# Kernel optimization log

Hardware: AMD Instinct MI355X
Metric: run time of the kernel (lower is better)

## Reference

```python
import jax, jax.numpy as jnp
import numpy as np

B = 1048576
IN, H = 16, 12


def _xavier(key, shape):
    fan_out, fan_in = shape
    lim = jnp.sqrt(6.0 / (fan_in + fan_out))
    return jax.random.uniform(key, shape, jnp.float32, -lim, lim)


def _lstm_cell_zero_state(x, W_ih, b_ih, b_hh):
    # PyTorch LSTMCell with h0=c0=0: h0 @ W_hh.T == 0, so W_hh drops out of
    # the forward math (its gradient is exactly zero); b_hh still contributes.
    gates = x @ W_ih.T + b_ih + b_hh          # [B, 4H]
    i, f, g, o = jnp.split(gates, 4, axis=-1)  # PyTorch gate order: i,f,g,o
    c = jax.nn.sigmoid(i) * jnp.tanh(g)        # f*c0 == 0
    h = jax.nn.sigmoid(o) * jnp.tanh(c)
    return h


def setup_inputs() -> dict:
    key = jax.random.key(0)
    ks = jax.random.split(key, 9)
    x = jax.random.normal(ks[0], (B, IN), jnp.float32)
    d = {"x": x}
    specs = [("1", IN), ("2", H), ("m", H), ("d", H)]
    for idx, (tag, in_dim) in enumerate(specs):
        kw, kb = jax.random.split(ks[idx + 1])
        d[f"W_ih{tag}"] = _xavier(kw, (4 * H, in_dim))
        kb1, kb2 = jax.random.split(kb)
        lim = 1.0 / np.sqrt(H)
        d[f"b_ih{tag}"] = jax.random.uniform(kb1, (4 * H,), jnp.float32, -lim, lim)
        d[f"b_hh{tag}"] = jax.random.uniform(kb2, (4 * H,), jnp.float32, -lim, lim)
    return d


def reference(x, W_ih1, b_ih1, b_hh1, W_ih2, b_ih2, b_hh2,
              W_ihm, b_ihm, b_hhm, W_ihd, b_ihd, b_hhd):
    h1 = jax.nn.relu(_lstm_cell_zero_state(x, W_ih1, b_ih1, b_hh1))
    h2 = jax.nn.selu(_lstm_cell_zero_state(h1, W_ih2, b_ih2, b_hh2))
    m = jnp.tanh(_lstm_cell_zero_state(h2, W_ihm, b_ihm, b_hhm))
    dv = jnp.tanh(_lstm_cell_zero_state(h2, W_ihd, b_ihd, b_hhd))
    return jnp.concatenate([m, dv], axis=0)  # [2B, H]
```

## Files before the change

### kernel.cpp

```cpp
#include <hip/hip_runtime.h>

#define L2E 1.4426950408889634f

typedef float  f32x4  __attribute__((ext_vector_type(4)));
typedef short  bf16x8 __attribute__((ext_vector_type(8)));

__device__ __forceinline__ float ex2(float x){ return __builtin_amdgcn_exp2f(x); }
__device__ __forceinline__ float rcpf_(float x){ return __builtin_amdgcn_rcpf(x); }
__device__ __forceinline__ unsigned short f2bf(float f){
    unsigned u = __float_as_uint(f);
    u = (u + 0x7FFFu + ((u >> 16) & 1u)) >> 16;
    return (unsigned short)u;
}
__device__ __forceinline__ float bf2f(unsigned short h){
    return __uint_as_float(((unsigned)h) << 16);
}

union FragCast { uint4 u; bf16x8 v; };

__device__ __forceinline__ float cell_act(f32x4 d){
    float ei = ex2(d.x), tg = ex2(d.y), eo = ex2(d.z);
    float rig = rcpf_((1.0f+ei)*(1.0f+tg));
    float c   = (1.0f-tg)*rig;
    float c2  = c*c;
    float num = c*(945.0f + c2*(105.0f + c2));
    float den = 945.0f + c2*(420.0f + 15.0f*c2);
    return num * rcpf_((1.0f+eo)*den);
}
__device__ __forceinline__ float tanh_pade(float x){
    float x2 = x*x;
    return x*(945.0f + x2*(105.0f + x2)) * rcpf_(945.0f + x2*(420.0f + 15.0f*x2));
}

__global__ void prep_kernel(
    const float* __restrict__ W1, const float* __restrict__ bi1, const float* __restrict__ bh1,
    const float* __restrict__ W2, const float* __restrict__ bi2, const float* __restrict__ bh2,
    const float* __restrict__ Wm, const float* __restrict__ bim, const float* __restrict__ bhm,
    const float* __restrict__ Wd, const float* __restrict__ bid, const float* __restrict__ bhd,
    unsigned short* __restrict__ wsA, float* __restrict__ wsB1)
{
    const float* Ws[4]  = {W1, W2, Wm, Wd};
    const float* bis[4] = {bi1, bi2, bim, bid};
    const float* bhs[4] = {bh1, bh2, bhm, bhd};
    const int goff[3] = {0, 24, 36};

    int t = blockIdx.x * blockDim.x + threadIdx.x;
    if (t < 12288) {
        int fragid = t >> 9;
        int le = t & 511;
        int l  = le >> 3, e = le & 7;
        int p  = fragid & 1;
        int cmb = fragid >> 1;
        int c  = cmb / 3, mb = cmb % 3;
        int m  = l & 15, kg = l >> 4;
        int k  = kg * 8 + e;
        int gr = mb * 16 + m;
        int t3 = gr & 3, j = gr >> 2;
        int K  = (c == 0) ? 16 : 12;
        int col = (k < 16) ? k : (k - 16);
        unsigned short outv = 0;
        if (t3 < 3) {
            float gscv = (t3 == 1) ? (-2.0f * L2E) : (-L2E);
            bool biasslot = (c > 0) && (k < 16) && (col == 12 || col == 13);
            float full = 0.0f;
            if (col < K)        full = gscv * Ws[c][(goff[t3] + j) * K + col];
            else if (biasslot)  full = gscv * (bis[c][goff[t3] + j] + bhs[c][goff[t3] + j]);
            if (p == 0) {
                unsigned short hi = f2bf(full);
                outv = (biasslot && col == 13) ? f2bf(full - bf2f(hi)) : hi;
            } else {
                if (k < 16 && col < K) {
                    unsigned short hi = f2bf(full);
                    outv = f2bf(full - bf2f(hi));
                }
            }
        }
        wsA[t] = outv;
    } else if (t < 13056) {
        int u = t - 12288;
        int r = u & 3, v = u >> 2;
        int l = v & 63, mb = v >> 6;
        float val = 0.0f;
        if (r < 3) {
            int gr = mb * 16 + ((l >> 4) * 4) + r;
            int j  = gr >> 2;
            float gscv = (r == 1) ? (-2.0f * L2E) : (-L2E);
            val = gscv * (bis[0][goff[r] + j] + bhs[0][goff[r] + j]);
        }
        wsB1[u] = val;
    }
}

__global__ __launch_bounds__(256, 2) void dynnet_kernel(
    const float* __restrict__ x, const unsigned short* __restrict__ wsA,
    const float* __restrict__ wsB1, float* __restrict__ out, int nrows)
{
    __shared__ __align__(16) unsigned short lds[4][2][640];
    const int lane = threadIdx.x & 63;
    const int wid  = threadIdx.x >> 6;
    const int n    = lane & 15;
    const int kg   = lane >> 4;
    unsigned short* bufA = &lds[wid][0][0];
    unsigned short* bufB = &lds[wid][1][0];

    if (lane < 16) {
        *(unsigned long long*)&bufA[lane*40 + 12] = 0x3F803F80ULL;
        *(unsigned long long*)&bufA[lane*40 + 28] = 0ULL;
        *(unsigned long long*)&bufB[lane*40 + 12] = 0x3F803F80ULL;
        *(unsigned long long*)&bufB[lane*40 + 28] = 0ULL;
    }

    bf16x8 Afr[24];
    const uint4* wsA4 = (const uint4*)wsA;
#pragma unroll
    for (int f = 0; f < 24; ++f) {
        FragCast fc; fc.u = wsA4[f*64 + lane]; Afr[f] = fc.v;
    }
    f32x4 b1[3];
    const float4* wsB14 = (const float4*)wsB1;
#pragma unroll
    for (int mb = 0; mb < 3; ++mb) {
        float4 tb = wsB14[mb*64 + lane];
        b1[mb] = (f32x4){tb.x, tb.y, tb.z, tb.w};
    }

    const int ntiles = nrows >> 4;
    const int nw = gridDim.x * 4;
    int tile = blockIdx.x * 4 + wid;
    if (tile >= ntiles) return;

    float4 xv0, xv1;
    {
        const float* xp = x + (size_t)(tile*16 + n)*16 + (kg & 1)*8;
        xv0 = ((const float4*)xp)[0];
        xv1 = ((const float4*)xp)[1];
    }

    const f32x4 z4 = {0.f, 0.f, 0.f, 0.f};

    for (; tile < ntiles; tile += nw) {
        float xe[8] = {xv0.x,xv0.y,xv0.z,xv0.w, xv1.x,xv1.y,xv1.z,xv1.w};
        bf16x8 xB;
        const bool wantlo = (kg >= 2);
#pragma unroll
        for (int e = 0; e < 8; ++e) {
            unsigned short hi = f2bf(xe[e]);
            unsigned short v  = wantlo ? f2bf(xe[e] - bf2f(hi)) : hi;
            xB[e] = (short)v;
        }

        const int row0 = tile*16 + n;

#pragma unroll
        for (int mb = 0; mb < 3; ++mb) {
            f32x4 acc = __builtin_amdgcn_mfma_f32_16x16x32_bf16(Afr[mb*2+0], xB, b1[mb], 0,0,0);
            acc       = __builtin_amdgcn_mfma_f32_16x16x32_bf16(Afr[mb*2+1], xB, acc,    0,0,0);
            float h = fmaxf(cell_act(acc), 0.0f);
            unsigned short hi = f2bf(h);
            unsigned short lo = f2bf(h - bf2f(hi));
            bufA[n*40 + (mb*4 + kg)]      = hi;
            bufA[n*40 + 16 + (mb*4 + kg)] = lo;
        }

        {
            int pt = tile + nw; if (pt > ntiles - 1) pt = ntiles - 1;
            const float* xp = x + (size_t)(pt*16 + n)*16 + (kg & 1)*8;
            xv0 = ((const float4*)xp)[0];
            xv1 = ((const float4*)xp)[1];
        }

        asm volatile("s_waitcnt lgkmcnt(0)" ::: "memory");
        FragCast f2c; f2c.u = *(const uint4*)&bufA[n*40 + kg*8];
        bf16x8 B2 = f2c.v;

#pragma unroll
        for (int mb = 0; mb < 3; ++mb) {
            f32x4 acc = __builtin_amdgcn_mfma_f32_16x16x32_bf16(Afr[6 + mb*2+0], B2, z4, 0,0,0);
            acc       = __builtin_amdgcn_mfma_f32_16x16x32_bf16(Afr[6 + mb*2+1], B2, acc, 0,0,0);
            float v = cell_act(acc);
            float ev = ex2(v * L2E);
            float s = (v > 0.0f) ? (1.0507009873554805f * v)
                                 : fmaf(ev, 1.7580993408473766f, -1.7580993408473766f);
            unsigned short hi = f2bf(s);
            unsigned short lo = f2bf(s - bf2f(hi));
            bufB[n*40 + (mb*4 + kg)]      = hi;
            bufB[n*40 + 16 + (mb*4 + kg)] = lo;
        }

        asm volatile("s_waitcnt lgkmcnt(0)" ::: "memory");
        FragCast f3c; f3c.u = *(const uint4*)&bufB[n*40 + kg*8];
        bf16x8 B3 = f3c.v;

        float* om = out + (size_t)row0 * 12;
        float* od = out + ((size_t)nrows + row0) * 12;
#pragma unroll
        for (int mb = 0; mb < 3; ++mb) {
            f32x4 am = __builtin_amdgcn_mfma_f32_16x16x32_bf16(Afr[12 + mb*2+0], B3, z4, 0,0,0);
            am       = __builtin_amdgcn_mfma_f32_16x16x32_bf16(Afr[12 + mb*2+1], B3, am, 0,0,0);
            f32x4 ad = __builtin_amdgcn_mfma_f32_16x16x32_bf16(Afr[18 + mb*2+0], B3, z4, 0,0,0);
            ad       = __builtin_amdgcn_mfma_f32_16x16x32_bf16(Afr[18 + mb*2+1], B3, ad, 0,0,0);
            om[mb*4 + kg] = tanh_pade(cell_act(am));
            od[mb*4 + kg] = tanh_pade(cell_act(ad));
        }
    }
}

extern "C" void kernel_launch(void* const* d_in, const int* in_sizes, int n_in,
                              void* d_out, int out_size, void* d_ws, size_t ws_size,
                              hipStream_t stream) {
    const float* x    = (const float*)d_in[0];
    const float* Wih1 = (const float*)d_in[1];
    const float* bih1 = (const float*)d_in[2];
    const float* bhh1 = (const float*)d_in[3];
    const float* Wih2 = (const float*)d_in[4];
    const float* bih2 = (const float*)d_in[5];
    const float* bhh2 = (const float*)d_in[6];
    const float* Wihm = (const float*)d_in[7];
    const float* bihm = (const float*)d_in[8];
    const float* bhhm = (const float*)d_in[9];
    const float* Wihd = (const float*)d_in[10];
    const float* bihd = (const float*)d_in[11];
    const float* bhhd = (const float*)d_in[12];
    float* out = (float*)d_out;

    unsigned short* wsA = (unsigned short*)d_ws;
    float* wsB1 = (float*)((char*)d_ws + 24576);

    prep_kernel<<<51, 256, 0, stream>>>(Wih1, bih1, bhh1, Wih2, bih2, bhh2,
                                        Wihm, bihm, bhhm, Wihd, bihd, bhhd,
                                        wsA, wsB1);

    int nrows = in_sizes[0] / 16;
    dynnet_kernel<<<2048, 256, 0, stream>>>(x, wsA, wsB1, out, nrows);
}
```

Baseline: 206.7 us.

## Interleave bf16 hi/lo split pairs and truncate high halves

Changes the K layout of the bf16 split-precision operands so each value's high and low parts sit next to each other. The high part is now plain truncation and the low part is the residual, so one packed 32-bit LDS store replaces two 16-bit stores. Each lane now loads a single float4 of x, where before it loaded two. The weight prep layout is reordered to match, and launch bounds move to 3 blocks per SM, which may limit registers and risk spills given the 24 held A fragments.

```diff
diff --git a/kernel.cpp b/kernel.cpp
--- a/kernel.cpp
+++ b/kernel.cpp
@@ -1,4 +1,5 @@
 #include <hip/hip_runtime.h>
+#include <hip/hip_bf16.h>
 
 #define L2E 1.4426950408889634f
 
@@ -8,15 +9,20 @@
 __device__ __forceinline__ float ex2(float x){ return __builtin_amdgcn_exp2f(x); }
 __device__ __forceinline__ float rcpf_(float x){ return __builtin_amdgcn_rcpf(x); }
 __device__ __forceinline__ unsigned short f2bf(float f){
-    unsigned u = __float_as_uint(f);
-    u = (u + 0x7FFFu + ((u >> 16) & 1u)) >> 16;
-    return (unsigned short)u;
+    return __builtin_bit_cast(unsigned short, __float2bfloat16(f));
 }
 __device__ __forceinline__ float bf2f(unsigned short h){
     return __uint_as_float(((unsigned)h) << 16);
 }
+__device__ __forceinline__ unsigned pack_hl(float v){
+    unsigned u   = __float_as_uint(v);
+    float    rem = v - __uint_as_float(u & 0xFFFF0000u);
+    unsigned lo  = f2bf(rem);
+    return (u >> 16) | (lo << 16);
+}
 
 union FragCast { uint4 u; bf16x8 v; };
+union BWords   { unsigned w[4]; bf16x8 v; };
 
 __device__ __forceinline__ float cell_act(f32x4 d){
     float ei = ex2(d.x), tg = ex2(d.y), eo = ex2(d.z);
@@ -57,22 +63,19 @@
         int gr = mb * 16 + m;
         int t3 = gr & 3, j = gr >> 2;
         int K  = (c == 0) ? 16 : 12;
-        int col = (k < 16) ? k : (k - 16);
+        int i  = k >> 1, odd = k & 1;
         unsigned short outv = 0;
         if (t3 < 3) {
             float gscv = (t3 == 1) ? (-2.0f * L2E) : (-L2E);
-            bool biasslot = (c > 0) && (k < 16) && (col == 12 || col == 13);
-            float full = 0.0f;
-            if (col < K)        full = gscv * Ws[c][(goff[t3] + j) * K + col];
-            else if (biasslot)  full = gscv * (bis[c][goff[t3] + j] + bhs[c][goff[t3] + j]);
-            if (p == 0) {
+            if (i < K) {
+                float full = gscv * Ws[c][(goff[t3] + j) * K + i];
                 unsigned short hi = f2bf(full);
-                outv = (biasslot && col == 13) ? f2bf(full - bf2f(hi)) : hi;
-            } else {
-                if (k < 16 && col < K) {
-                    unsigned short hi = f2bf(full);
-                    outv = f2bf(full - bf2f(hi));
-                }
+                if (p == 0) outv = hi;
+                else        outv = odd ? 0 : f2bf(full - bf2f(hi));
+            } else if (c > 0 && (k == 24 || k == 25) && p == 0) {
+                float b = gscv * (bis[c][goff[t3] + j] + bhs[c][goff[t3] + j]);
+                unsigned short hi = f2bf(b);
+                outv = (k == 24) ? hi : f2bf(b - bf2f(hi));
             }
         }
         wsA[t] = outv;
@@ -91,7 +94,7 @@
     }
 }
 
-__global__ __launch_bounds__(256, 2) void dynnet_kernel(
+__global__ __launch_bounds__(256, 3) void dynnet_kernel(
     const float* __restrict__ x, const unsigned short* __restrict__ wsA,
     const float* __restrict__ wsB1, float* __restrict__ out, int nrows)
 {
@@ -104,9 +107,9 @@
     unsigned short* bufB = &lds[wid][1][0];
 
     if (lane < 16) {
-        *(unsigned long long*)&bufA[lane*40 + 12] = 0x3F803F80ULL;
+        *(unsigned long long*)&bufA[lane*40 + 24] = 0x000000003F803F80ULL;
         *(unsigned long long*)&bufA[lane*40 + 28] = 0ULL;
-        *(unsigned long long*)&bufB[lane*40 + 12] = 0x3F803F80ULL;
+        *(unsigned long long*)&bufB[lane*40 + 24] = 0x000000003F803F80ULL;
         *(unsigned long long*)&bufB[lane*40 + 28] = 0ULL;
     }
 
@@ -129,25 +132,15 @@
     int tile = blockIdx.x * 4 + wid;
     if (tile >= ntiles) return;
 
-    float4 xv0, xv1;
-    {
-        const float* xp = x + (size_t)(tile*16 + n)*16 + (kg & 1)*8;
-        xv0 = ((const float4*)xp)[0];
-        xv1 = ((const float4*)xp)[1];
-    }
+    float4 xv = ((const float4*)(x + (size_t)(tile*16 + n)*16))[kg];
 
     const f32x4 z4 = {0.f, 0.f, 0.f, 0.f};
 
     for (; tile < ntiles; tile += nw) {
-        float xe[8] = {xv0.x,xv0.y,xv0.z,xv0.w, xv1.x,xv1.y,xv1.z,xv1.w};
-        bf16x8 xB;
-        const bool wantlo = (kg >= 2);
-#pragma unroll
-        for (int e = 0; e < 8; ++e) {
-            unsigned short hi = f2bf(xe[e]);
-            unsigned short v  = wantlo ? f2bf(xe[e] - bf2f(hi)) : hi;
-            xB[e] = (short)v;
-        }
+        BWords xb;
+        xb.w[0] = pack_hl(xv.x); xb.w[1] = pack_hl(xv.y);
+        xb.w[2] = pack_hl(xv.z); xb.w[3] = pack_hl(xv.w);
+        bf16x8 xB = xb.v;
 
         const int row0 = tile*16 + n;
 
@@ -156,17 +149,12 @@
             f32x4 acc = __builtin_amdgcn_mfma_f32_16x16x32_bf16(Afr[mb*2+0], xB, b1[mb], 0,0,0);
             acc       = __builtin_amdgcn_mfma_f32_16x16x32_bf16(Afr[mb*2+1], xB, acc,    0,0,0);
             float h = fmaxf(cell_act(acc), 0.0f);
-            unsigned short hi = f2bf(h);
-            unsigned short lo = f2bf(h - bf2f(hi));
-            bufA[n*40 + (mb*4 + kg)]      = hi;
-            bufA[n*40 + 16 + (mb*4 + kg)] = lo;
+            *(unsigned*)&bufA[n*40 + (mb*4 + kg)*2] = pack_hl(h);
         }
 
         {
             int pt = tile + nw; if (pt > ntiles - 1) pt = ntiles - 1;
-            const float* xp = x + (size_t)(pt*16 + n)*16 + (kg & 1)*8;
-            xv0 = ((const float4*)xp)[0];
-            xv1 = ((const float4*)xp)[1];
+            xv = ((const float4*)(x + (size_t)(pt*16 + n)*16))[kg];
         }
 
         asm volatile("s_waitcnt lgkmcnt(0)" ::: "memory");
@@ -181,10 +169,7 @@
             float ev = ex2(v * L2E);
             float s = (v > 0.0f) ? (1.0507009873554805f * v)
                                  : fmaf(ev, 1.7580993408473766f, -1.7580993408473766f);
-            unsigned short hi = f2bf(s);
-            unsigned short lo = f2bf(s - bf2f(hi));
-            bufB[n*40 + (mb*4 + kg)]      = hi;
-            bufB[n*40 + 16 + (mb*4 + kg)] = lo;
+            *(unsigned*)&bufB[n*40 + (mb*4 + kg)*2] = pack_hl(s);
         }
 
         asm volatile("s_waitcnt lgkmcnt(0)" ::: "memory");
```

Measured after the change: 205.0 us. Within noise of the previous version (-0.9%).
